# Optimization experiments

Hardware: AMD Instinct MI355X
Metric: run time of the kernel (lower is better)

The kernel has to match this reference:

```python
import jax, jax.numpy as jnp
import numpy as np

HIDDEN = 256


def setup_inputs() -> dict:
    key = jax.random.key(0)
    ks = jax.random.split(key, 6)
    b, c_len, q_len, h = 32, 1024, 128, HIDDEN
    # Xavier-uniform bounds for the learned weights
    lim_vec = float(np.sqrt(6.0 / (h + 1)))      # (h, 1) weights
    lim_cq = float(np.sqrt(6.0 / (1 + h)))       # (1, 1, h) weight
    return {
        "context": jax.random.normal(ks[0], (b, c_len, h), dtype=jnp.float32),
        "query": jax.random.normal(ks[1], (b, q_len, h), dtype=jnp.float32),
        "c_mask": jnp.zeros((b, c_len), dtype=bool),
        "q_mask": jnp.zeros((b, q_len), dtype=bool),
        "c_weight": jax.random.uniform(ks[2], (h, 1), jnp.float32, -lim_vec, lim_vec),
        "q_weight": jax.random.uniform(ks[3], (h, 1), jnp.float32, -lim_vec, lim_vec),
        "cq_weight": jax.random.uniform(ks[4], (1, 1, h), jnp.float32, -lim_cq, lim_cq),
        "bias": jnp.zeros((1,), dtype=jnp.float32),
    }


def reference(context, query, c_mask, q_mask, c_weight, q_weight, cq_weight, bias):
    # Trilinear similarity: S[b,i,j] = c_i.w_c + q_j.w_q + (c_i * w_cq).q_j + bias
    s0 = context @ c_weight                                  # (b, c, 1)
    s1 = jnp.swapaxes(query @ q_weight, 1, 2)                # (b, 1, q)
    s2 = jnp.einsum('bch,bqh->bcq', context * cq_weight, query)
    S = s0 + s1 + s2 + bias                                  # (b, c, q)

    S_bar = jax.nn.softmax(S, axis=1)       # softmax over context axis
    S_bar_bar = jax.nn.softmax(S, axis=2)   # softmax over query axis

    A = jnp.einsum('bcq,bqh->bch', S, query)  # note: raw S, as in source
    B = jnp.einsum('bcq,bkq,bkh->bch', S_bar, S_bar_bar, context)

    return jnp.concatenate([context, A, context * A, context * B], axis=2)
```

## Files before the change

kernel.cpp:

```cpp
#include <hip/hip_runtime.h>
#include <cstdint>
#include <cstddef>

#define BATCH 32
#define CLEN  1024
#define QLEN  128
#define HID   256

typedef __attribute__((ext_vector_type(8))) short bf16x8;
typedef __attribute__((ext_vector_type(4))) float f32x4;

#define MFMA(a, b, c) __builtin_amdgcn_mfma_f32_16x16x32_bf16((a), (b), (c), 0, 0, 0)

__device__ __forceinline__ ushort f2b(float f) {
    union { float f; uint u; } v; v.f = f;
    uint r = (v.u + 0x7fffu + ((v.u >> 16) & 1u)) >> 16;
    return (ushort)r;
}
__device__ __forceinline__ float b2f(ushort u) {
    union { uint u; float f; } v; v.u = ((uint)u) << 16;
    return v.f;
}

__global__ __launch_bounds__(256) void prep_kernel(
    const float* __restrict__ context, const float* __restrict__ query,
    const float* __restrict__ cw, const float* __restrict__ qw,
    const float* __restrict__ cqw,
    ushort* __restrict__ ctxT, ushort* __restrict__ mcB,
    ushort* __restrict__ qB, ushort* __restrict__ qT,
    float* __restrict__ cdot, float* __restrict__ qdot)
{
    __shared__ ushort lds[64][258];
    int bid = blockIdx.x;
    int t = threadIdx.x;
    int r = t >> 2, qd = t & 3;
    if (bid < 512) {
        int b = bid >> 4, c0 = (bid & 15) * 64;
        const float* src = context + ((size_t)(b * CLEN + c0 + r)) * HID;
        ushort* mcr = mcB + ((size_t)(b * CLEN + c0 + r)) * HID;
        float dot = 0.f;
        #pragma unroll
        for (int j = 0; j < 16; j++) {
            int h = j * 16 + qd * 4;
            float4 v  = *reinterpret_cast<const float4*>(src + h);
            float4 w  = *reinterpret_cast<const float4*>(cw + h);
            float4 wc = *reinterpret_cast<const float4*>(cqw + h);
            dot += v.x * w.x + v.y * w.y + v.z * w.z + v.w * w.w;
            uint p0 = (uint)f2b(v.x) | ((uint)f2b(v.y) << 16);
            uint p1 = (uint)f2b(v.z) | ((uint)f2b(v.w) << 16);
            *reinterpret_cast<uint*>(&lds[r][h])     = p0;
            *reinterpret_cast<uint*>(&lds[r][h + 2]) = p1;
            uint2 mc;
            mc.x = (uint)f2b(v.x * wc.x) | ((uint)f2b(v.y * wc.y) << 16);
            mc.y = (uint)f2b(v.z * wc.z) | ((uint)f2b(v.w * wc.w) << 16);
            *reinterpret_cast<uint2*>(mcr + h) = mc;
        }
        dot += __shfl_xor(dot, 1);
        dot += __shfl_xor(dot, 2);
        if (qd == 0) cdot[b * CLEN + c0 + r] = dot;
        __syncthreads();
        ushort* dst = ctxT + ((size_t)(b * HID + t)) * CLEN + c0;
        #pragma unroll
        for (int j = 0; j < 8; j++) {
            uint4 w;
            w.x = (uint)lds[j*8+0][t] | ((uint)lds[j*8+1][t] << 16);
            w.y = (uint)lds[j*8+2][t] | ((uint)lds[j*8+3][t] << 16);
            w.z = (uint)lds[j*8+4][t] | ((uint)lds[j*8+5][t] << 16);
            w.w = (uint)lds[j*8+6][t] | ((uint)lds[j*8+7][t] << 16);
            *reinterpret_cast<uint4*>(dst + j * 8) = w;
        }
    } else {
        int bb = bid - 512;
        int b = bb >> 1, q0 = (bb & 1) * 64;
        const float* src = query + ((size_t)(b * QLEN + q0 + r)) * HID;
        ushort* qBr = qB + ((size_t)(b * QLEN + q0 + r)) * HID;
        float dot = 0.f;
        #pragma unroll
        for (int j = 0; j < 16; j++) {
            int h = j * 16 + qd * 4;
            float4 v = *reinterpret_cast<const float4*>(src + h);
            float4 w = *reinterpret_cast<const float4*>(qw + h);
            dot += v.x * w.x + v.y * w.y + v.z * w.z + v.w * w.w;
            uint p0 = (uint)f2b(v.x) | ((uint)f2b(v.y) << 16);
            uint p1 = (uint)f2b(v.z) | ((uint)f2b(v.w) << 16);
            *reinterpret_cast<uint*>(&lds[r][h])     = p0;
            *reinterpret_cast<uint*>(&lds[r][h + 2]) = p1;
            uint2 pk; pk.x = p0; pk.y = p1;
            *reinterpret_cast<uint2*>(qBr + h) = pk;
        }
        dot += __shfl_xor(dot, 1);
        dot += __shfl_xor(dot, 2);
        if (qd == 0) qdot[b * QLEN + q0 + r] = dot;
        __syncthreads();
        ushort* dst = qT + ((size_t)(b * HID + t)) * QLEN + q0;
        #pragma unroll
        for (int j = 0; j < 8; j++) {
            uint4 w;
            w.x = (uint)lds[j*8+0][t] | ((uint)lds[j*8+1][t] << 16);
            w.y = (uint)lds[j*8+2][t] | ((uint)lds[j*8+3][t] << 16);
            w.z = (uint)lds[j*8+4][t] | ((uint)lds[j*8+5][t] << 16);
            w.w = (uint)lds[j*8+6][t] | ((uint)lds[j*8+7][t] << 16);
            *reinterpret_cast<uint4*>(dst + j * 8) = w;
        }
    }
}

__global__ __launch_bounds__(256) void s_kernel(
    const ushort* __restrict__ mcB, const ushort* __restrict__ qB,
    const float* __restrict__ cdot, const float* __restrict__ qdot,
    const float* __restrict__ bias,
    ushort* __restrict__ S, ushort* __restrict__ P2T)
{
    __shared__ float ldsS[64][132];
    __shared__ float ldsM[64], ldsR[64];
    int ct = blockIdx.x, b = blockIdx.y;
    int c0 = ct * 64;
    int t = threadIdx.x;
    int w = t >> 6, L = t & 63, g = L >> 4, ln = L & 15;
    int wr = w >> 1, wc = w & 1;

    f32x4 acc[2][4];
    #pragma unroll
    for (int mi = 0; mi < 2; mi++)
        #pragma unroll
        for (int ni = 0; ni < 4; ni++) acc[mi][ni] = (f32x4){0.f, 0.f, 0.f, 0.f};

    const ushort* aBase = mcB + ((size_t)(b * CLEN + c0 + wr * 32)) * HID;
    const ushort* qBb   = qB + ((size_t)(b * QLEN + wc * 64)) * HID;

    #pragma unroll 2
    for (int kk = 0; kk < 8; kk++) {
        int k = kk * 32 + g * 8;
        bf16x8 a[2], bq[4];
        #pragma unroll
        for (int mi = 0; mi < 2; mi++)
            a[mi] = *reinterpret_cast<const bf16x8*>(aBase + (size_t)(mi * 16 + ln) * HID + k);
        #pragma unroll
        for (int ni = 0; ni < 4; ni++)
            bq[ni] = *reinterpret_cast<const bf16x8*>(qBb + (size_t)(ni * 16 + ln) * HID + k);
        #pragma unroll
        for (int mi = 0; mi < 2; mi++)
            #pragma unroll
            for (int ni = 0; ni < 4; ni++)
                acc[mi][ni] = MFMA(a[mi], bq[ni], acc[mi][ni]);
    }

    float bv = bias[0];
    float qdv[4];
    #pragma unroll
    for (int ni = 0; ni < 4; ni++) qdv[ni] = qdot[b * QLEN + wc * 64 + ni * 16 + ln];
    #pragma unroll
    for (int mi = 0; mi < 2; mi++)
        #pragma unroll
        for (int r = 0; r < 4; r++) {
            int row = wr * 32 + mi * 16 + g * 4 + r;
            float cd = cdot[b * CLEN + c0 + row] + bv;
            #pragma unroll
            for (int ni = 0; ni < 4; ni++)
                ldsS[row][wc * 64 + ni * 16 + ln] = acc[mi][ni][r] + cd + qdv[ni];
        }
    __syncthreads();
    {
        int row = t >> 2, qs = (t & 3) * 32;
        float4 vr[8];
        float m = -1e30f;
        #pragma unroll
        for (int j = 0; j < 8; j++) {
            vr[j] = *reinterpret_cast<const float4*>(&ldsS[row][qs + j * 4]);
            m = fmaxf(m, fmaxf(fmaxf(vr[j].x, vr[j].y), fmaxf(vr[j].z, vr[j].w)));
        }
        m = fmaxf(m, __shfl_xor(m, 1));
        m = fmaxf(m, __shfl_xor(m, 2));
        float s = 0.f;
        #pragma unroll
        for (int j = 0; j < 8; j++)
            s += __expf(vr[j].x - m) + __expf(vr[j].y - m) +
                 __expf(vr[j].z - m) + __expf(vr[j].w - m);
        s += __shfl_xor(s, 1);
        s += __shfl_xor(s, 2);
        if ((t & 3) == 0) { ldsM[row] = m; ldsR[row] = 1.0f / s; }
    }
    __syncthreads();
    {
        const size_t Sbase = ((size_t)b * CLEN + c0) * QLEN;
        #pragma unroll
        for (int i = 0; i < 8; i++) {
            int flat = t + 256 * i;
            int q4 = flat & 31, c = flat >> 5;
            float4 v = *reinterpret_cast<const float4*>(&ldsS[c][q4 * 4]);
            uint2 pk;
            pk.x = (uint)f2b(v.x) | ((uint)f2b(v.y) << 16);
            pk.y = (uint)f2b(v.z) | ((uint)f2b(v.w) << 16);
            *reinterpret_cast<uint2*>(&S[Sbase + (size_t)c * QLEN + q4 * 4]) = pk;
        }
    }
    {
        int q = t >> 1, half = t & 1;
        ushort* dst = P2T + ((size_t)b * QLEN + q) * CLEN + c0 + half * 32;
        #pragma unroll
        for (int jo = 0; jo < 4; jo++) {
            uint pk[4];
            #pragma unroll
            for (int l = 0; l < 4; l++) {
                int c0l = half * 32 + jo * 8 + l * 2;
                float p0 = __expf(ldsS[c0l][q]     - ldsM[c0l])     * ldsR[c0l];
                float p1 = __expf(ldsS[c0l + 1][q] - ldsM[c0l + 1]) * ldsR[c0l + 1];
                pk[l] = (uint)f2b(p0) | ((uint)f2b(p1) << 16);
            }
            uint4 wv; wv.x = pk[0]; wv.y = pk[1]; wv.z = pk[2]; wv.w = pk[3];
            *reinterpret_cast<uint4*>(dst + jo * 8) = wv;
        }
    }
}

__global__ __launch_bounds__(256) void colstats_kernel(
    const ushort* __restrict__ S, float* __restrict__ colmax, float* __restrict__ colsumr)
{
    __shared__ float red[8][32];
    __shared__ float Mv[32];
    int q0 = blockIdx.x * 32, b = blockIdx.y;
    int t = threadIdx.x, q = t & 31, cs = t >> 5;
    const ushort* p = S + (size_t)b * CLEN * QLEN + (size_t)cs * 128 * QLEN + q0 + q;
    float m0 = -1e30f, m1 = -1e30f, m2 = -1e30f, m3 = -1e30f;
    #pragma unroll 8
    for (int i = 0; i < 128; i += 4) {
        m0 = fmaxf(m0, b2f(p[(size_t)(i + 0) * QLEN]));
        m1 = fmaxf(m1, b2f(p[(size_t)(i + 1) * QLEN]));
        m2 = fmaxf(m2, b2f(p[(size_t)(i + 2) * QLEN]));
        m3 = fmaxf(m3, b2f(p[(size_t)(i + 3) * QLEN]));
    }
    red[cs][q] = fmaxf(fmaxf(m0, m1), fmaxf(m2, m3));
    __syncthreads();
    if (t < 32) {
        float mm = red[0][t];
        #pragma unroll
        for (int j = 1; j < 8; j++) mm = fmaxf(mm, red[j][t]);
        Mv[t] = mm;
    }
    __syncthreads();
    float M = Mv[q];
    float s0 = 0.f, s1 = 0.f, s2 = 0.f, s3 = 0.f;
    #pragma unroll 8
    for (int i = 0; i < 128; i += 4) {
        s0 += __expf(b2f(p[(size_t)(i + 0) * QLEN]) - M);
        s1 += __expf(b2f(p[(size_t)(i + 1) * QLEN]) - M);
        s2 += __expf(b2f(p[(size_t)(i + 2) * QLEN]) - M);
        s3 += __expf(b2f(p[(size_t)(i + 3) * QLEN]) - M);
    }
    __syncthreads();
    red[cs][q] = (s0 + s1) + (s2 + s3);
    __syncthreads();
    if (t < 32) {
        float ss = 0.f;
        #pragma unroll
        for (int j = 0; j < 8; j++) ss += red[j][t];
        colmax[b * QLEN + q0 + t]  = Mv[t];
        colsumr[b * QLEN + q0 + t] = 1.0f / ss;
    }
}

__global__ __launch_bounds__(256) void t_kernel(
    const ushort* __restrict__ ctxT, const ushort* __restrict__ P2T,
    float* __restrict__ Tpart)
{
    int x = blockIdx.x, b = blockIdx.y;
    int h0 = (x >> 1) * 64, ks = x & 1;
    int t = threadIdx.x;
    int w = t >> 6, L = t & 63, g = L >> 4, ln = L & 15;
    int wr = w >> 1, wc = w & 1;

    f32x4 acc[2][4];
    #pragma unroll
    for (int mi = 0; mi < 2; mi++)
        #pragma unroll
        for (int ni = 0; ni < 4; ni++) acc[mi][ni] = (f32x4){0.f, 0.f, 0.f, 0.f};

    const ushort* aB = ctxT + ((size_t)(b * HID + h0 + wr * 32)) * CLEN + ks * 512;
    const ushort* bB = P2T + ((size_t)(b * QLEN + wc * 64)) * CLEN + ks * 512;

    #pragma unroll 2
    for (int kk = 0; kk < 16; kk++) {
        int k = kk * 32 + g * 8;
        bf16x8 a[2], bq[4];
        #pragma unroll
        for (int mi = 0; mi < 2; mi++)
            a[mi] = *reinterpret_cast<const bf16x8*>(aB + (size_t)(mi * 16 + ln) * CLEN + k);
        #pragma unroll
        for (int ni = 0; ni < 4; ni++)
            bq[ni] = *reinterpret_cast<const bf16x8*>(bB + (size_t)(ni * 16 + ln) * CLEN + k);
        #pragma unroll
        for (int mi = 0; mi < 2; mi++)
            #pragma unroll
            for (int ni = 0; ni < 4; ni++)
                acc[mi][ni] = MFMA(a[mi], bq[ni], acc[mi][ni]);
    }
    float* dst = Tpart + (size_t)ks * (BATCH * HID * QLEN);
    #pragma unroll
    for (int mi = 0; mi < 2; mi++)
        #pragma unroll
        for (int ni = 0; ni < 4; ni++)
            #pragma unroll
            for (int r = 0; r < 4; r++) {
                int h = h0 + wr * 32 + mi * 16 + g * 4 + r;
                int q = wc * 64 + ni * 16 + ln;
                dst[((size_t)b * HID + h) * QLEN + q] = acc[mi][ni][r];
            }
}

__global__ __launch_bounds__(256) void t_reduce_kernel(
    const float* __restrict__ Tpart, ushort* __restrict__ Tt)
{
    int gid = blockIdx.x * 256 + threadIdx.x;
    const float4* p = reinterpret_cast<const float4*>(Tpart);
    float4 a = p[gid];
    float4 b = p[gid + 262144];
    float4 r = make_float4(a.x + b.x, a.y + b.y, a.z + b.z, a.w + b.w);
    uint2 pk;
    pk.x = (uint)f2b(r.x) | ((uint)f2b(r.y) << 16);
    pk.y = (uint)f2b(r.z) | ((uint)f2b(r.w) << 16);
    *reinterpret_cast<uint2*>(Tt + (size_t)gid * 4) = pk;
}

__global__ __launch_bounds__(256) void ab_out_kernel(
    const ushort* __restrict__ S, const ushort* __restrict__ qT,
    const ushort* __restrict__ Tt, const float* __restrict__ context,
    const float* __restrict__ colmax, const float* __restrict__ colsumr,
    float* __restrict__ out)
{
    __shared__ float ldsT[128][68];
    int x = blockIdx.x, b = blockIdx.y;
    int c0 = (x >> 2) * 128, h0 = (x & 3) * 64;
    int t = threadIdx.x;
    int w = t >> 6, L = t & 63, g = L >> 4, ln = L & 15;
    int wr = w >> 1, wc = w & 1;

    f32x4 accA[4][2], accB[4][2];
    #pragma unroll
    for (int mi = 0; mi < 4; mi++)
        #pragma unroll
        for (int ni = 0; ni < 2; ni++) {
            accA[mi][ni] = (f32x4){0.f, 0.f, 0.f, 0.f};
            accB[mi][ni] = (f32x4){0.f, 0.f, 0.f, 0.f};
        }

    const ushort* Srow = S + ((size_t)(b * CLEN + c0 + wr * 64)) * QLEN;
    const ushort* qTb  = qT + ((size_t)(b * HID + h0 + wc * 32)) * QLEN;
    const ushort* TtB  = Tt + ((size_t)(b * HID + h0 + wc * 32)) * QLEN;
    const float* cmB = colmax + b * QLEN;
    const float* crB = colsumr + b * QLEN;

    #pragma unroll
    for (int kk = 0; kk < 4; kk++) {
        int k = kk * 32 + g * 8;
        float4 cm0 = *reinterpret_cast<const float4*>(cmB + k);
        float4 cm1 = *reinterpret_cast<const float4*>(cmB + k + 4);
        float4 cr0 = *reinterpret_cast<const float4*>(crB + k);
        float4 cr1 = *reinterpret_cast<const float4*>(crB + k + 4);
        float cmv[8] = {cm0.x, cm0.y, cm0.z, cm0.w, cm1.x, cm1.y, cm1.z, cm1.w};
        float crv[8] = {cr0.x, cr0.y, cr0.z, cr0.w, cr1.x, cr1.y, cr1.z, cr1.w};
        bf16x8 sa[4], pa[4];
        #pragma unroll
        for (int mi = 0; mi < 4; mi++) {
            sa[mi] = *reinterpret_cast<const bf16x8*>(Srow + (size_t)(mi * 16 + ln) * QLEN + k);
            bf16x8 pv;
            #pragma unroll
            for (int i = 0; i < 8; i++) {
                float f = b2f((ushort)sa[mi][i]);
                pv[i] = (short)f2b(__expf(f - cmv[i]) * crv[i]);
            }
            pa[mi] = pv;
        }
        bf16x8 bq[2], bt[2];
        #pragma unroll
        for (int ni = 0; ni < 2; ni++) {
            bq[ni] = *reinterpret_cast<const bf16x8*>(qTb + (size_t)(ni * 16 + ln) * QLEN + k);
            bt[ni] = *reinterpret_cast<const bf16x8*>(TtB + (size_t)(ni * 16 + ln) * QLEN + k);
        }
        #pragma unroll
        for (int mi = 0; mi < 4; mi++)
            #pragma unroll
            for (int ni = 0; ni < 2; ni++) {
                accA[mi][ni] = MFMA(sa[mi], bq[ni], accA[mi][ni]);
                accB[mi][ni] = MFMA(pa[mi], bt[ni], accB[mi][ni]);
            }
    }

    #pragma unroll
    for (int mi = 0; mi < 4; mi++)
        #pragma unroll
        for (int ni = 0; ni < 2; ni++)
            #pragma unroll
            for (int r = 0; r < 4; r++)
                ldsT[wr * 64 + mi * 16 + g * 4 + r][wc * 32 + ni * 16 + ln] = accA[mi][ni][r];
    __syncthreads();
    #pragma unroll
    for (int i = 0; i < 8; i++) {
        int flat = t + 256 * i;
        int h4 = flat & 15, c = flat >> 4;
        float4 av = *reinterpret_cast<const float4*>(&ldsT[c][h4 * 4]);
        float4 cv = *reinterpret_cast<const float4*>(
            context + ((size_t)(b * CLEN + c0 + c)) * HID + h0 + h4 * 4);
        size_t o = ((size_t)(b * CLEN + c0 + c)) * 1024 + h0 + h4 * 4;
        *reinterpret_cast<float4*>(&out[o]) = cv;
        *reinterpret_cast<float4*>(&out[o + 256]) = av;
        *reinterpret_cast<float4*>(&out[o + 512]) =
            make_float4(cv.x * av.x, cv.y * av.y, cv.z * av.z, cv.w * av.w);
    }
    __syncthreads();
    #pragma unroll
    for (int mi = 0; mi < 4; mi++)
        #pragma unroll
        for (int ni = 0; ni < 2; ni++)
            #pragma unroll
            for (int r = 0; r < 4; r++)
                ldsT[wr * 64 + mi * 16 + g * 4 + r][wc * 32 + ni * 16 + ln] = accB[mi][ni][r];
    __syncthreads();
    #pragma unroll
    for (int i = 0; i < 8; i++) {
        int flat = t + 256 * i;
        int h4 = flat & 15, c = flat >> 4;
        float4 bvv = *reinterpret_cast<const float4*>(&ldsT[c][h4 * 4]);
        float4 cv = *reinterpret_cast<const float4*>(
            context + ((size_t)(b * CLEN + c0 + c)) * HID + h0 + h4 * 4);
        size_t o = ((size_t)(b * CLEN + c0 + c)) * 1024 + h0 + h4 * 4;
        *reinterpret_cast<float4*>(&out[o + 768]) =
            make_float4(cv.x * bvv.x, cv.y * bvv.y, cv.z * bvv.z, cv.w * bvv.w);
    }
}

extern "C" void kernel_launch(void* const* d_in, const int* in_sizes, int n_in,
                              void* d_out, int out_size, void* d_ws, size_t ws_size,
                              hipStream_t stream)
{
    (void)in_sizes; (void)n_in; (void)out_size; (void)ws_size;
    const float* context   = (const float*)d_in[0];
    const float* query     = (const float*)d_in[1];
    const float* c_weight  = (const float*)d_in[4];
    const float* q_weight  = (const float*)d_in[5];
    const float* cq_weight = (const float*)d_in[6];
    const float* bias      = (const float*)d_in[7];
    float* out = (float*)d_out;
    char* wsb  = (char*)d_ws;

    ushort* ctxT = (ushort*)(wsb);
    ushort* mcB  = (ushort*)(wsb + 16777216);
    ushort* qB   = (ushort*)(wsb + 33554432);
    ushort* qT   = (ushort*)(wsb + 35651584);
    ushort* S    = (ushort*)(wsb + 37748736);
    ushort* P2T  = (ushort*)(wsb + 46137344);
    ushort* Tt   = (ushort*)(wsb + 54525952);
    float*  Tpart = (float*)(wsb + 56623104);
    float*  cdot  = (float*)(wsb + 65011712);
    float*  qdot  = cdot + 32768;
    float*  colmax  = qdot + 4096;
    float*  colsumr = colmax + 4096;

    prep_kernel<<<576, 256, 0, stream>>>(context, query, c_weight, q_weight,
                                         cq_weight, ctxT, mcB, qB, qT, cdot, qdot);
    s_kernel<<<dim3(16, 32), 256, 0, stream>>>(mcB, qB, cdot, qdot, bias, S, P2T);
    colstats_kernel<<<dim3(4, 32), 256, 0, stream>>>(S, colmax, colsumr);
    t_kernel<<<dim3(8, 32), 256, 0, stream>>>(ctxT, P2T, Tpart);
    t_reduce_kernel<<<1024, 256, 0, stream>>>(Tpart, Tt);
    ab_out_kernel<<<dim3(32, 32), 256, 0, stream>>>(S, qT, Tt, context,
                                                    colmax, colsumr, out);
}
```

Measured before the change: 111.8 us.

## Materialize unnormalized column-softmax P1 and fold reciprocal sums into T

The column-stats kernel is rewritten to use vectorized 16-byte loads and wave shuffles. It now also writes exp(S - colmax) as a bf16 tensor P1u. The 1/colsum normalization is moved out of the per-element softmax and applied to T in the reduce kernel, since it depends only on q. As a result ab_out no longer recomputes exp per element and just loads P1u. The cost is an extra 8 MB bf16 write and read in exchange for removing redundant exp work in the big output kernel.

Result: slower. 120.3 us (+7.6%).

```diff
diff --git a/kernel.cpp b/kernel.cpp
--- a/kernel.cpp
+++ b/kernel.cpp
@@ -213,49 +213,74 @@
     }
 }
 
-__global__ __launch_bounds__(256) void colstats_kernel(
-    const ushort* __restrict__ S, float* __restrict__ colmax, float* __restrict__ colsumr)
-{
-    __shared__ float red[8][32];
-    __shared__ float Mv[32];
-    int q0 = blockIdx.x * 32, b = blockIdx.y;
-    int t = threadIdx.x, q = t & 31, cs = t >> 5;
-    const ushort* p = S + (size_t)b * CLEN * QLEN + (size_t)cs * 128 * QLEN + q0 + q;
-    float m0 = -1e30f, m1 = -1e30f, m2 = -1e30f, m3 = -1e30f;
-    #pragma unroll 8
-    for (int i = 0; i < 128; i += 4) {
-        m0 = fmaxf(m0, b2f(p[(size_t)(i + 0) * QLEN]));
-        m1 = fmaxf(m1, b2f(p[(size_t)(i + 1) * QLEN]));
-        m2 = fmaxf(m2, b2f(p[(size_t)(i + 2) * QLEN]));
-        m3 = fmaxf(m3, b2f(p[(size_t)(i + 3) * QLEN]));
-    }
-    red[cs][q] = fmaxf(fmaxf(m0, m1), fmaxf(m2, m3));
-    __syncthreads();
-    if (t < 32) {
-        float mm = red[0][t];
-        #pragma unroll
-        for (int j = 1; j < 8; j++) mm = fmaxf(mm, red[j][t]);
-        Mv[t] = mm;
-    }
-    __syncthreads();
-    float M = Mv[q];
-    float s0 = 0.f, s1 = 0.f, s2 = 0.f, s3 = 0.f;
-    #pragma unroll 8
-    for (int i = 0; i < 128; i += 4) {
-        s0 += __expf(b2f(p[(size_t)(i + 0) * QLEN]) - M);
-        s1 += __expf(b2f(p[(size_t)(i + 1) * QLEN]) - M);
-        s2 += __expf(b2f(p[(size_t)(i + 2) * QLEN]) - M);
-        s3 += __expf(b2f(p[(size_t)(i + 3) * QLEN]) - M);
-    }
-    __syncthreads();
-    red[cs][q] = (s0 + s1) + (s2 + s3);
-    __syncthreads();
-    if (t < 32) {
-        float ss = 0.f;
-        #pragma unroll
-        for (int j = 0; j < 8; j++) ss += red[j][t];
-        colmax[b * QLEN + q0 + t]  = Mv[t];
-        colsumr[b * QLEN + q0 + t] = 1.0f / ss;
+__global__ __launch_bounds__(256) void colp1_kernel(
+    const ushort* __restrict__ S, ushort* __restrict__ P1u,
+    float* __restrict__ colmax, float* __restrict__ colsumr)
+{
+    __shared__ float red[4][2][8];
+    __shared__ float MS[16];
+    int qc = blockIdx.x, b = blockIdx.y;
+    int q0 = qc * 16;
+    int t = threadIdx.x;
+    int qh = t & 1, cg = t >> 1;
+    int w = t >> 6, L = t & 63;
+    const ushort* base = S + (size_t)b * CLEN * QLEN + q0 + qh * 8;
+    float vm[8];
+    #pragma unroll
+    for (int j = 0; j < 8; j++) vm[j] = -1e30f;
+    #pragma unroll
+    for (int i = 0; i < 8; i++) {
+        bf16x8 v = *reinterpret_cast<const bf16x8*>(base + (size_t)(cg + 128 * i) * QLEN);
+        #pragma unroll
+        for (int j = 0; j < 8; j++) vm[j] = fmaxf(vm[j], b2f((ushort)v[j]));
+    }
+    #pragma unroll
+    for (int off = 2; off <= 32; off <<= 1)
+        #pragma unroll
+        for (int j = 0; j < 8; j++) vm[j] = fmaxf(vm[j], __shfl_xor(vm[j], off, 64));
+    if (L < 2) {
+        #pragma unroll
+        for (int j = 0; j < 8; j++) red[w][L][j] = vm[j];
+    }
+    __syncthreads();
+    if (t < 16) {
+        int j = t & 7, qq = t >> 3;
+        float m = fmaxf(fmaxf(red[0][qq][j], red[1][qq][j]),
+                        fmaxf(red[2][qq][j], red[3][qq][j]));
+        MS[qq * 8 + j] = m;
+        colmax[b * QLEN + q0 + qq * 8 + j] = m;
+    }
+    __syncthreads();
+    float M[8], sum[8];
+    #pragma unroll
+    for (int j = 0; j < 8; j++) { M[j] = MS[qh * 8 + j]; sum[j] = 0.f; }
+    ushort* dstb = P1u + (size_t)b * CLEN * QLEN + q0 + qh * 8;
+    #pragma unroll
+    for (int i = 0; i < 8; i++) {
+        size_t off = (size_t)(cg + 128 * i) * QLEN;
+        bf16x8 v = *reinterpret_cast<const bf16x8*>(base + off);
+        bf16x8 o;
+        #pragma unroll
+        for (int j = 0; j < 8; j++) {
+            float e = __expf(b2f((ushort)v[j]) - M[j]);
+            sum[j] += e;
+            o[j] = (short)f2b(e);
+        }
+        *reinterpret_cast<bf16x8*>(dstb + off) = o;
+    }
+    #pragma unroll
+    for (int off = 2; off <= 32; off <<= 1)
+        #pragma unroll
+        for (int j = 0; j < 8; j++) sum[j] += __shfl_xor(sum[j], off, 64);
+    if (L < 2) {
+        #pragma unroll
+        for (int j = 0; j < 8; j++) red[w][L][j] = sum[j];
+    }
+    __syncthreads();
+    if (t < 16) {
+        int j = t & 7, qq = t >> 3;
+        float s = red[0][qq][j] + red[1][qq][j] + red[2][qq][j] + red[3][qq][j];
+        colsumr[b * QLEN + q0 + qq * 8 + j] = 1.0f / s;
     }
 }
 
@@ -308,13 +333,17 @@
 }
 
 __global__ __launch_bounds__(256) void t_reduce_kernel(
-    const float* __restrict__ Tpart, ushort* __restrict__ Tt)
+    const float* __restrict__ Tpart, const float* __restrict__ colsumr,
+    ushort* __restrict__ Tt)
 {
     int gid = blockIdx.x * 256 + threadIdx.x;
+    int b = gid >> 13, q4 = (gid & 31) * 4;
     const float4* p = reinterpret_cast<const float4*>(Tpart);
+    float4 cr = *reinterpret_cast<const float4*>(colsumr + b * QLEN + q4);
     float4 a = p[gid];
-    float4 b = p[gid + 262144];
-    float4 r = make_float4(a.x + b.x, a.y + b.y, a.z + b.z, a.w + b.w);
+    float4 bb = p[gid + 262144];
+    float4 r = make_float4((a.x + bb.x) * cr.x, (a.y + bb.y) * cr.y,
+                           (a.z + bb.z) * cr.z, (a.w + bb.w) * cr.w);
     uint2 pk;
     pk.x = (uint)f2b(r.x) | ((uint)f2b(r.y) << 16);
     pk.y = (uint)f2b(r.z) | ((uint)f2b(r.w) << 16);
@@ -322,10 +351,9 @@
 }
 
 __global__ __launch_bounds__(256) void ab_out_kernel(
-    const ushort* __restrict__ S, const ushort* __restrict__ qT,
-    const ushort* __restrict__ Tt, const float* __restrict__ context,
-    const float* __restrict__ colmax, const float* __restrict__ colsumr,
-    float* __restrict__ out)
+    const ushort* __restrict__ S, const ushort* __restrict__ P1u,
+    const ushort* __restrict__ qT, const ushort* __restrict__ Tt,
+    const float* __restrict__ context, float* __restrict__ out)
 {
     __shared__ float ldsT[128][68];
     int x = blockIdx.x, b = blockIdx.y;
@@ -343,34 +371,20 @@
             accB[mi][ni] = (f32x4){0.f, 0.f, 0.f, 0.f};
         }
 
-    const ushort* Srow = S + ((size_t)(b * CLEN + c0 + wr * 64)) * QLEN;
-    const ushort* qTb  = qT + ((size_t)(b * HID + h0 + wc * 32)) * QLEN;
-    const ushort* TtB  = Tt + ((size_t)(b * HID + h0 + wc * 32)) * QLEN;
-    const float* cmB = colmax + b * QLEN;
-    const float* crB = colsumr + b * QLEN;
+    const ushort* Srow  = S + ((size_t)(b * CLEN + c0 + wr * 64)) * QLEN;
+    const ushort* P1row = P1u + ((size_t)(b * CLEN + c0 + wr * 64)) * QLEN;
+    const ushort* qTb   = qT + ((size_t)(b * HID + h0 + wc * 32)) * QLEN;
+    const ushort* TtB   = Tt + ((size_t)(b * HID + h0 + wc * 32)) * QLEN;
 
     #pragma unroll
     for (int kk = 0; kk < 4; kk++) {
         int k = kk * 32 + g * 8;
-        float4 cm0 = *reinterpret_cast<const float4*>(cmB + k);
-        float4 cm1 = *reinterpret_cast<const float4*>(cmB + k + 4);
-        float4 cr0 = *reinterpret_cast<const float4*>(crB + k);
-        float4 cr1 = *reinterpret_cast<const float4*>(crB + k + 4);
-        float cmv[8] = {cm0.x, cm0.y, cm0.z, cm0.w, cm1.x, cm1.y, cm1.z, cm1.w};
-        float crv[8] = {cr0.x, cr0.y, cr0.z, cr0.w, cr1.x, cr1.y, cr1.z, cr1.w};
-        bf16x8 sa[4], pa[4];
+        bf16x8 sa[4], pa[4], bq[2], bt[2];
         #pragma unroll
         for (int mi = 0; mi < 4; mi++) {
-            sa[mi] = *reinterpret_cast<const bf16x8*>(Srow + (size_t)(mi * 16 + ln) * QLEN + k);
-            bf16x8 pv;
-            #pragma unroll
-            for (int i = 0; i < 8; i++) {
-                float f = b2f((ushort)sa[mi][i]);
-                pv[i] = (short)f2b(__expf(f - cmv[i]) * crv[i]);
-            }
-            pa[mi] = pv;
-        }
-        bf16x8 bq[2], bt[2];
+            sa[mi] = *reinterpret_cast<const bf16x8*>(Srow  + (size_t)(mi * 16 + ln) * QLEN + k);
+            pa[mi] = *reinterpret_cast<const bf16x8*>(P1row + (size_t)(mi * 16 + ln) * QLEN + k);
+        }
         #pragma unroll
         for (int ni = 0; ni < 2; ni++) {
             bq[ni] = *reinterpret_cast<const bf16x8*>(qTb + (size_t)(ni * 16 + ln) * QLEN + k);
@@ -448,19 +462,19 @@
     ushort* qT   = (ushort*)(wsb + 35651584);
     ushort* S    = (ushort*)(wsb + 37748736);
     ushort* P2T  = (ushort*)(wsb + 46137344);
-    ushort* Tt   = (ushort*)(wsb + 54525952);
-    float*  Tpart = (float*)(wsb + 56623104);
-    float*  cdot  = (float*)(wsb + 65011712);
-    float*  qdot  = cdot + 32768;
+    ushort* P1u  = (ushort*)(wsb + 54525952);
+    ushort* Tt   = (ushort*)(wsb + 62914560);
+    float*  Tpart = (float*)(wsb + 65011712);
+    float*  cdot  = (float*)(wsb + 73400320);
+    float*  qdot    = cdot + 32768;
     float*  colmax  = qdot + 4096;
     float*  colsumr = colmax + 4096;
 
     prep_kernel<<<576, 256, 0, stream>>>(context, query, c_weight, q_weight,
                                          cq_weight, ctxT, mcB, qB, qT, cdot, qdot);
     s_kernel<<<dim3(16, 32), 256, 0, stream>>>(mcB, qB, cdot, qdot, bias, S, P2T);
-    colstats_kernel<<<dim3(4, 32), 256, 0, stream>>>(S, colmax, colsumr);
+    colp1_kernel<<<dim3(8, 32), 256, 0, stream>>>(S, P1u, colmax, colsumr);
     t_kernel<<<dim3(8, 32), 256, 0, stream>>>(ctxT, P2T, Tpart);
-    t_reduce_kernel<<<1024, 256, 0, stream>>>(Tpart, Tt);
-    ab_out_kernel<<<dim3(32, 32), 256, 0, stream>>>(S, qT, Tt, context,
-                                                    colmax, colsumr, out);
-}
+    t_reduce_kernel<<<1024, 256, 0, stream>>>(Tpart, colsumr, Tt);
+    ab_out_kernel<<<dim3(32, 32), 256, 0, stream>>>(S, P1u, qT, Tt, context, out);
+}
```
